# Kernel tuning notes

Measured on AMD Instinct MI355X. Metric: run time of the kernel, lower is better.

## Reference

```python
import jax, jax.numpy as jnp
import numpy as np

T, B, D, H = 200, 4096, 64, 64


def setup_inputs() -> dict:
    key = jax.random.key(0)
    k1, k2, k3, k4, k5, k6, k7 = jax.random.split(key, 7)
    x = jax.random.normal(k1, (T, B, D), dtype=jnp.float32)
    weights = jax.random.uniform(k2, (T, B, 1), dtype=jnp.float32)
    # descending lengths in [1, T], mimicking packed-sequence sorting
    lengths = jnp.flip(jnp.sort(jax.random.randint(k3, (B,), 1, T + 1, dtype=jnp.int32)))
    s = 1.0 / np.sqrt(H)
    W_ih = jax.random.uniform(k4, (3 * H, D), minval=-s, maxval=s, dtype=jnp.float32)
    W_hh = jax.random.uniform(k5, (3 * H, H), minval=-s, maxval=s, dtype=jnp.float32)
    b_ih = jax.random.uniform(k6, (3 * H,), minval=-s, maxval=s, dtype=jnp.float32)
    b_hh = jax.random.uniform(k7, (3 * H,), minval=-s, maxval=s, dtype=jnp.float32)
    return {"x": x, "weights": weights, "lengths": lengths,
            "W_ih": W_ih, "W_hh": W_hh, "b_ih": b_ih, "b_hh": b_hh}


def reference(x, weights, lengths, W_ih, W_hh, b_ih, b_hh):
    # Padded-equivalent of the packed AUGRU loop: rows beyond a sequence's
    # length keep a frozen hidden state and emit zeros (outputs were zero-init).
    hidden = W_hh.shape[1]
    mask = (jnp.arange(x.shape[0])[:, None] < lengths[None, :])  # [T, B]

    def step(h, inp):
        xt, wt, mt = inp  # [B,D], [B,1], [B]
        gi = xt @ W_ih.T + b_ih          # [B, 3H]
        gh = h @ W_hh.T + b_hh           # [B, 3H]
        i_r, i_z, i_n = jnp.split(gi, 3, axis=1)
        h_r, h_z, h_n = jnp.split(gh, 3, axis=1)
        reset_gate = jax.nn.sigmoid(i_r + h_r)
        update_gate = jax.nn.sigmoid(i_z + h_z)
        new_state = jnp.tanh(i_n + reset_gate * h_n)
        update_gate = wt * update_gate
        hy = (1.0 - update_gate) * h + update_gate * new_state
        m = mt[:, None]
        h_next = jnp.where(m, hy, h)
        out = jnp.where(m, hy, jnp.zeros_like(hy))
        return h_next, out

    h0 = jnp.zeros((x.shape[1], hidden), dtype=x.dtype)
    _, outputs = jax.lax.scan(step, h0, (x, weights, mask))
    return outputs  # [T, B, H], padded-equivalent of PackedSequence data
```

## Files before the change

kernel.cpp:

```cpp
#include <hip/hip_runtime.h>
#include <hip/hip_bf16.h>


#define T_STEPS 200
#define BATCH   4096

typedef __attribute__((ext_vector_type(8))) __bf16 bf16x8;
typedef __attribute__((ext_vector_type(4))) float  f32x4;

__global__ __launch_bounds__(256) void augru_kernel(
    const float* __restrict__ x,
    const float* __restrict__ wts,
    const int*   __restrict__ lengths,
    const float* __restrict__ W_ih,
    const float* __restrict__ W_hh,
    const float* __restrict__ b_ih,
    const float* __restrict__ b_hh,
    float* __restrict__ out)
{
    const int tid   = threadIdx.x;
    const int wave  = tid >> 6;
    const int lane  = tid & 63;
    const int l15   = lane & 15;
    const int lhi   = lane >> 4;
    const int rbase = blockIdx.x * 16;
    const int j     = wave * 16 + l15;

    __shared__ __bf16 hbuf[2][16 * 64];
    __shared__ int smax;

    if (tid == 0) smax = 1;
    for (int i = tid; i < 1024; i += 256) hbuf[0][i] = (__bf16)0.0f;

    bf16x8 wih[3][2], whh[3][2];
#pragma unroll
    for (int g = 0; g < 3; ++g) {
        const int grow = (g * 4 + wave) * 16 + l15;
#pragma unroll
        for (int c = 0; c < 2; ++c) {
            const float* pih = W_ih + grow * 64 + c * 32 + lhi * 8;
            const float* phh = W_hh + grow * 64 + c * 32 + lhi * 8;
#pragma unroll
            for (int i = 0; i < 8; ++i) {
                wih[g][c][i] = (__bf16)pih[i];
                whh[g][c][i] = (__bf16)phh[i];
            }
        }
    }

    const float bir = b_ih[j],       bhr = b_hh[j];
    const float biz = b_ih[64 + j],  bhz = b_hh[64 + j];
    const float bin = b_ih[128 + j], bhn = b_hh[128 + j];

    int   row[4], len[4];
    float hprev[4];
#pragma unroll
    for (int i = 0; i < 4; ++i) {
        row[i]   = rbase + lhi * 4 + i;
        len[i]   = lengths[row[i]];
        hprev[i] = 0.0f;
    }
    {
        int ml = max(max(len[0], len[1]), max(len[2], len[3]));
        __syncthreads();
        atomicMax(&smax, ml);
    }

    f32x4 xn0, xn1, xn2, xn3; float wtn[4];
    {
        const float* p = x + (size_t)(rbase + l15) * 64 + lhi * 8;
        xn0 = *(const f32x4*)(p);        xn1 = *(const f32x4*)(p + 4);
        xn2 = *(const f32x4*)(p + 32);   xn3 = *(const f32x4*)(p + 32 + 4);
#pragma unroll
        for (int i = 0; i < 4; ++i) wtn[i] = wts[row[i]];
    }

    __syncthreads();
    const int maxlen = smax;

    for (int t = 0; t < maxlen; ++t) {
        f32x4 xc0 = xn0, xc1 = xn1, xc2 = xn2, xc3 = xn3;
        float wt[4];
#pragma unroll
        for (int i = 0; i < 4; ++i) wt[i] = wtn[i];

        const int tn = (t + 1 < T_STEPS) ? t + 1 : t;
        {
            const float* p = x + (size_t)tn * (BATCH * 64)
                               + (size_t)(rbase + l15) * 64 + lhi * 8;
            xn0 = *(const f32x4*)(p);        xn1 = *(const f32x4*)(p + 4);
            xn2 = *(const f32x4*)(p + 32);   xn3 = *(const f32x4*)(p + 32 + 4);
#pragma unroll
            for (int i = 0; i < 4; ++i) wtn[i] = wts[(size_t)tn * BATCH + row[i]];
        }

        bf16x8 xf0, xf1;
#pragma unroll
        for (int i = 0; i < 4; ++i) {
            xf0[i]     = (__bf16)xc0[i];
            xf0[i + 4] = (__bf16)xc1[i];
            xf1[i]     = (__bf16)xc2[i];
            xf1[i + 4] = (__bf16)xc3[i];
        }

        f32x4 gi0 = {0,0,0,0}, gi1 = {0,0,0,0}, gi2 = {0,0,0,0};
        gi0 = __builtin_amdgcn_mfma_f32_16x16x32_bf16(xf0, wih[0][0], gi0, 0,0,0);
        gi1 = __builtin_amdgcn_mfma_f32_16x16x32_bf16(xf0, wih[1][0], gi1, 0,0,0);
        gi2 = __builtin_amdgcn_mfma_f32_16x16x32_bf16(xf0, wih[2][0], gi2, 0,0,0);
        gi0 = __builtin_amdgcn_mfma_f32_16x16x32_bf16(xf1, wih[0][1], gi0, 0,0,0);
        gi1 = __builtin_amdgcn_mfma_f32_16x16x32_bf16(xf1, wih[1][1], gi1, 0,0,0);
        gi2 = __builtin_amdgcn_mfma_f32_16x16x32_bf16(xf1, wih[2][1], gi2, 0,0,0);

        const int pr = t & 1;
        bf16x8 hf0, hf1;
        {
            const int base = l15 * 64;
            const int sw   = (l15 & 7) << 3;
            hf0 = *(const bf16x8*)&hbuf[pr][base + ((lhi * 8)      ^ sw)];
            hf1 = *(const bf16x8*)&hbuf[pr][base + ((32 + lhi * 8) ^ sw)];
        }

        f32x4 gh0 = {0,0,0,0}, gh1 = {0,0,0,0}, gh2 = {0,0,0,0};
        gh0 = __builtin_amdgcn_mfma_f32_16x16x32_bf16(hf0, whh[0][0], gh0, 0,0,0);
        gh1 = __builtin_amdgcn_mfma_f32_16x16x32_bf16(hf0, whh[1][0], gh1, 0,0,0);
        gh2 = __builtin_amdgcn_mfma_f32_16x16x32_bf16(hf0, whh[2][0], gh2, 0,0,0);
        gh0 = __builtin_amdgcn_mfma_f32_16x16x32_bf16(hf1, whh[0][1], gh0, 0,0,0);
        gh1 = __builtin_amdgcn_mfma_f32_16x16x32_bf16(hf1, whh[1][1], gh1, 0,0,0);
        gh2 = __builtin_amdgcn_mfma_f32_16x16x32_bf16(hf1, whh[2][1], gh2, 0,0,0);

        const int pw = (t + 1) & 1;
        float* outp = out + (size_t)t * (BATCH * 64);
#pragma unroll
        for (int i = 0; i < 4; ++i) {
            const float sr = (gi0[i] + bir) + (gh0[i] + bhr);
            const float sz = (gi1[i] + biz) + (gh1[i] + bhz);
            const float in_ = gi2[i] + bin;
            const float hn  = gh2[i] + bhn;
            const float r = 1.0f / (1.0f + __expf(-sr));
            const float z = 1.0f / (1.0f + __expf(-sz));
            const float v = in_ + r * hn;
            const float n = 1.0f - 2.0f / (1.0f + __expf(2.0f * v));
            const float u  = wt[i] * z;
            const float hy = (1.0f - u) * hprev[i] + u * n;
            const bool act = (t < len[i]);
            const float hnew = act ? hy : hprev[i];
            hprev[i] = hnew;
            __builtin_nontemporal_store(act ? hy : 0.0f,
                                        outp + (size_t)row[i] * 64 + j);
            const int lrow = lhi * 4 + i;
            hbuf[pw][(lrow * 64 + j) ^ ((lrow & 7) << 3)] = (__bf16)hnew;
        }
        __syncthreads();
    }

    {
        const f32x4 z4 = {0, 0, 0, 0};
        for (int t = maxlen; t < T_STEPS; ++t) {
            float* p = out + (size_t)t * (BATCH * 64) + (size_t)rbase * 64 + tid * 4;
            __builtin_nontemporal_store(z4, (f32x4*)p);
        }
    }
}

extern "C" void kernel_launch(void* const* d_in, const int* in_sizes, int n_in,
                              void* d_out, int out_size, void* d_ws, size_t ws_size,
                              hipStream_t stream) {
    const float* x    = (const float*)d_in[0];
    const float* wts  = (const float*)d_in[1];
    const int*   len  = (const int*)  d_in[2];
    const float* W_ih = (const float*)d_in[3];
    const float* W_hh = (const float*)d_in[4];
    const float* b_ih = (const float*)d_in[5];
    const float* b_hh = (const float*)d_in[6];
    float* outp = (float*)d_out;

    dim3 grid(BATCH / 16), block(256);
    augru_kernel<<<grid, block, 0, stream>>>(x, wts, len, W_ih, W_hh, b_ih, b_hh, outp);
}
```

Measured before the change: 511.9 us.

## Prefetch x two steps ahead, merge gate accumulators, use fast reciprocals and raw barrier

Deepens the x/weight prefetch from one to two timesteps using double register sets and a loop unrolled by two. The input and hidden projections for the r and z gates now accumulate into the same MFMA accumulator, with the biases pre-summed, which removes some VALU adds. Division is replaced with the hardware reciprocal approximation. __syncthreads is replaced by an explicit lgkmcnt wait plus s_barrier wrapped in sched_barriers, meant to avoid waiting on outstanding global loads at each step. The trade-offs are higher register pressure and slightly reduced numerical precision.

```diff
diff --git a/kernel.cpp b/kernel.cpp
--- a/kernel.cpp
+++ b/kernel.cpp
@@ -7,6 +7,8 @@
 
 typedef __attribute__((ext_vector_type(8))) __bf16 bf16x8;
 typedef __attribute__((ext_vector_type(4))) float  f32x4;
+
+#define MFMA16(a, b, c) __builtin_amdgcn_mfma_f32_16x16x32_bf16((a), (b), (c), 0, 0, 0)
 
 __global__ __launch_bounds__(256) void augru_kernel(
     const float* __restrict__ x,
@@ -48,8 +50,8 @@
         }
     }
 
-    const float bir = b_ih[j],       bhr = b_hh[j];
-    const float biz = b_ih[64 + j],  bhz = b_hh[64 + j];
+    const float brsum = b_ih[j] + b_hh[j];
+    const float bzsum = b_ih[64 + j] + b_hh[64 + j];
     const float bin = b_ih[128 + j], bhn = b_hh[128 + j];
 
     int   row[4], len[4];
@@ -66,51 +68,27 @@
         atomicMax(&smax, ml);
     }
 
-    f32x4 xn0, xn1, xn2, xn3; float wtn[4];
-    {
-        const float* p = x + (size_t)(rbase + l15) * 64 + lhi * 8;
-        xn0 = *(const f32x4*)(p);        xn1 = *(const f32x4*)(p + 4);
-        xn2 = *(const f32x4*)(p + 32);   xn3 = *(const f32x4*)(p + 32 + 4);
+    auto load_x = [&](int t, f32x4& a0, f32x4& a1, f32x4& a2, f32x4& a3) {
+        const float* p = x + (size_t)t * (BATCH * 64)
+                           + (size_t)(rbase + l15) * 64 + lhi * 8;
+        a0 = *(const f32x4*)(p);        a1 = *(const f32x4*)(p + 4);
+        a2 = *(const f32x4*)(p + 32);   a3 = *(const f32x4*)(p + 32 + 4);
+    };
+    auto load_w = [&](int t, float (&w4)[4]) {
 #pragma unroll
-        for (int i = 0; i < 4; ++i) wtn[i] = wts[row[i]];
-    }
+        for (int i = 0; i < 4; ++i) w4[i] = wts[(size_t)t * BATCH + row[i]];
+    };
+
+    f32x4 A0, A1, A2, A3, B0, B1, B2, B3;
+    float wtA[4], wtB[4];
+    load_x(0, A0, A1, A2, A3); load_w(0, wtA);
+    load_x(1, B0, B1, B2, B3); load_w(1, wtB);
 
     __syncthreads();
     const int maxlen = smax;
 
-    for (int t = 0; t < maxlen; ++t) {
-        f32x4 xc0 = xn0, xc1 = xn1, xc2 = xn2, xc3 = xn3;
-        float wt[4];
-#pragma unroll
-        for (int i = 0; i < 4; ++i) wt[i] = wtn[i];
-
-        const int tn = (t + 1 < T_STEPS) ? t + 1 : t;
-        {
-            const float* p = x + (size_t)tn * (BATCH * 64)
-                               + (size_t)(rbase + l15) * 64 + lhi * 8;
-            xn0 = *(const f32x4*)(p);        xn1 = *(const f32x4*)(p + 4);
-            xn2 = *(const f32x4*)(p + 32);   xn3 = *(const f32x4*)(p + 32 + 4);
-#pragma unroll
-            for (int i = 0; i < 4; ++i) wtn[i] = wts[(size_t)tn * BATCH + row[i]];
-        }
-
-        bf16x8 xf0, xf1;
-#pragma unroll
-        for (int i = 0; i < 4; ++i) {
-            xf0[i]     = (__bf16)xc0[i];
-            xf0[i + 4] = (__bf16)xc1[i];
-            xf1[i]     = (__bf16)xc2[i];
-            xf1[i + 4] = (__bf16)xc3[i];
-        }
-
-        f32x4 gi0 = {0,0,0,0}, gi1 = {0,0,0,0}, gi2 = {0,0,0,0};
-        gi0 = __builtin_amdgcn_mfma_f32_16x16x32_bf16(xf0, wih[0][0], gi0, 0,0,0);
-        gi1 = __builtin_amdgcn_mfma_f32_16x16x32_bf16(xf0, wih[1][0], gi1, 0,0,0);
-        gi2 = __builtin_amdgcn_mfma_f32_16x16x32_bf16(xf0, wih[2][0], gi2, 0,0,0);
-        gi0 = __builtin_amdgcn_mfma_f32_16x16x32_bf16(xf1, wih[0][1], gi0, 0,0,0);
-        gi1 = __builtin_amdgcn_mfma_f32_16x16x32_bf16(xf1, wih[1][1], gi1, 0,0,0);
-        gi2 = __builtin_amdgcn_mfma_f32_16x16x32_bf16(xf1, wih[2][1], gi2, 0,0,0);
-
+    auto do_step = [&](int t, f32x4& a0, f32x4& a1, f32x4& a2, f32x4& a3,
+                       float (&wtc)[4]) {
         const int pr = t & 1;
         bf16x8 hf0, hf1;
         {
@@ -119,29 +97,47 @@
             hf0 = *(const bf16x8*)&hbuf[pr][base + ((lhi * 8)      ^ sw)];
             hf1 = *(const bf16x8*)&hbuf[pr][base + ((32 + lhi * 8) ^ sw)];
         }
+        bf16x8 xf0, xf1;
+#pragma unroll
+        for (int i = 0; i < 4; ++i) {
+            xf0[i]     = (__bf16)a0[i];
+            xf0[i + 4] = (__bf16)a1[i];
+            xf1[i]     = (__bf16)a2[i];
+            xf1[i + 4] = (__bf16)a3[i];
+        }
+        float wt[4];
+#pragma unroll
+        for (int i = 0; i < 4; ++i) wt[i] = wtc[i];
 
-        f32x4 gh0 = {0,0,0,0}, gh1 = {0,0,0,0}, gh2 = {0,0,0,0};
-        gh0 = __builtin_amdgcn_mfma_f32_16x16x32_bf16(hf0, whh[0][0], gh0, 0,0,0);
-        gh1 = __builtin_amdgcn_mfma_f32_16x16x32_bf16(hf0, whh[1][0], gh1, 0,0,0);
-        gh2 = __builtin_amdgcn_mfma_f32_16x16x32_bf16(hf0, whh[2][0], gh2, 0,0,0);
-        gh0 = __builtin_amdgcn_mfma_f32_16x16x32_bf16(hf1, whh[0][1], gh0, 0,0,0);
-        gh1 = __builtin_amdgcn_mfma_f32_16x16x32_bf16(hf1, whh[1][1], gh1, 0,0,0);
-        gh2 = __builtin_amdgcn_mfma_f32_16x16x32_bf16(hf1, whh[2][1], gh2, 0,0,0);
+        const int tn = (t + 2 < T_STEPS) ? t + 2 : T_STEPS - 1;
+        load_x(tn, a0, a1, a2, a3);
+        load_w(tn, wtc);
+
+        f32x4 accR = {0,0,0,0}, accZ = {0,0,0,0};
+        f32x4 giN  = {0,0,0,0}, ghN  = {0,0,0,0};
+        accR = MFMA16(xf0, wih[0][0], accR);
+        accR = MFMA16(xf1, wih[0][1], accR);
+        accZ = MFMA16(xf0, wih[1][0], accZ);
+        accZ = MFMA16(xf1, wih[1][1], accZ);
+        giN  = MFMA16(xf0, wih[2][0], giN);
+        giN  = MFMA16(xf1, wih[2][1], giN);
+        accR = MFMA16(hf0, whh[0][0], accR);
+        accR = MFMA16(hf1, whh[0][1], accR);
+        accZ = MFMA16(hf0, whh[1][0], accZ);
+        accZ = MFMA16(hf1, whh[1][1], accZ);
+        ghN  = MFMA16(hf0, whh[2][0], ghN);
+        ghN  = MFMA16(hf1, whh[2][1], ghN);
 
         const int pw = (t + 1) & 1;
         float* outp = out + (size_t)t * (BATCH * 64);
 #pragma unroll
         for (int i = 0; i < 4; ++i) {
-            const float sr = (gi0[i] + bir) + (gh0[i] + bhr);
-            const float sz = (gi1[i] + biz) + (gh1[i] + bhz);
-            const float in_ = gi2[i] + bin;
-            const float hn  = gh2[i] + bhn;
-            const float r = 1.0f / (1.0f + __expf(-sr));
-            const float z = 1.0f / (1.0f + __expf(-sz));
-            const float v = in_ + r * hn;
-            const float n = 1.0f - 2.0f / (1.0f + __expf(2.0f * v));
+            const float r = __builtin_amdgcn_rcpf(1.0f + __expf(-(accR[i] + brsum)));
+            const float z = __builtin_amdgcn_rcpf(1.0f + __expf(-(accZ[i] + bzsum)));
+            const float v = (giN[i] + bin) + r * (ghN[i] + bhn);
+            const float n = 1.0f - 2.0f * __builtin_amdgcn_rcpf(1.0f + __expf(2.0f * v));
             const float u  = wt[i] * z;
-            const float hy = (1.0f - u) * hprev[i] + u * n;
+            const float hy = hprev[i] + u * (n - hprev[i]);
             const bool act = (t < len[i]);
             const float hnew = act ? hy : hprev[i];
             hprev[i] = hnew;
@@ -150,7 +146,17 @@
             const int lrow = lhi * 4 + i;
             hbuf[pw][(lrow * 64 + j) ^ ((lrow & 7) << 3)] = (__bf16)hnew;
         }
-        __syncthreads();
+
+        asm volatile("s_waitcnt lgkmcnt(0)" ::: "memory");
+        __builtin_amdgcn_sched_barrier(0);
+        __builtin_amdgcn_s_barrier();
+        __builtin_amdgcn_sched_barrier(0);
+    };
+
+    for (int t = 0; t < maxlen; t += 2) {
+        do_step(t, A0, A1, A2, A3, wtA);
+        if (t + 1 < maxlen)
+            do_step(t + 1, B0, B1, B2, B3, wtB);
     }
 
     {
```

Measured after the change: 442.4 us. 1.16x faster.
